# Optimization experiments

Hardware: AMD Instinct MI355X
Metric: run time of the kernel (lower is better)

The kernel has to match this reference:

```python
import jax, jax.numpy as jnp
import numpy as np

B, DAYS, N, E = 2, 8, 10000, 80000
C_IN, C_OUT, H = 32, 32, 4
NEG_SLOPE = 0.2


def setup_inputs() -> dict:
    key = jax.random.key(0)
    ks = jax.random.split(key, 7)
    x = jax.random.randint(ks[0], (B, DAYS, N), 0, N)
    adjacency = jax.random.randint(ks[1], (2, E), 0, N)
    embedding = jax.random.normal(ks[2], (N, C_IN), dtype=jnp.float32)
    # GATConv linear: in_channels -> heads*out_channels
    W = jax.random.normal(ks[3], (C_IN, H * C_OUT), dtype=jnp.float32) / np.sqrt(C_IN)
    att_src = jax.random.normal(ks[4], (H, C_OUT), dtype=jnp.float32) / np.sqrt(C_OUT)
    att_dst = jax.random.normal(ks[5], (H, C_OUT), dtype=jnp.float32) / np.sqrt(C_OUT)
    bias = jnp.zeros((H * C_OUT,), dtype=jnp.float32)
    return {"x": x, "adjacency": adjacency, "embedding": embedding,
            "W": W, "att_src": att_src, "att_dst": att_dst, "bias": bias}


def _gat_forward(feat, src, dst, W, att_src, att_dst, bias):
    # feat: [G, N, C_IN]; same edge list shared across the G graphs
    G = feat.shape[0]
    xh = (feat @ W).reshape(G, N, H, C_OUT)              # [G,N,H,C]
    a_src = jnp.einsum('gnhc,hc->gnh', xh, att_src)       # [G,N,H]
    a_dst = jnp.einsum('gnhc,hc->gnh', xh, att_dst)
    alpha = a_src[:, src] + a_dst[:, dst]                 # [G,Et,H]
    alpha = jnp.where(alpha >= 0, alpha, NEG_SLOPE * alpha)

    def per_graph(al, msgs):
        # segment softmax over incoming edges of each dst node
        m = jax.ops.segment_max(al, dst, num_segments=N)  # [N,H]
        e = jnp.exp(al - m[dst])                          # [Et,H]
        s = jax.ops.segment_sum(e, dst, num_segments=N)
        w = e / (s[dst] + 1e-16)
        out = jax.ops.segment_sum(w[..., None] * msgs, dst, num_segments=N)
        return out                                        # [N,H,C]

    out = jax.vmap(per_graph)(alpha, xh[:, src])          # [G,N,H,C]
    return out.reshape(G, N, H * C_OUT) + bias


def reference(x, adjacency, embedding, W, att_src, att_dst, bias):
    Bd, Dd = x.shape[0], x.shape[1]
    feat = embedding[x].reshape(-1, N, C_IN)              # [G,N,C_IN]
    # GATConv default add_self_loops=True
    loops = jnp.arange(N, dtype=adjacency.dtype)
    src = jnp.concatenate([adjacency[0], loops])
    dst = jnp.concatenate([adjacency[1], loops])
    out = _gat_forward(feat, src, dst, W, att_src, att_dst, bias)
    return out.reshape(Bd, Dd, -1)
```

## Files before the change

kernel.cpp:

```cpp
#include <hip/hip_runtime.h>
#include <hip/hip_bf16.h>
#include <math.h>

#define C_IN 32
#define H 4
#define C_OUT 32
#define HC (H * C_OUT)
#define NEG_SLOPE 0.2f
#define CSR_STRIDE 64

typedef float v2f __attribute__((ext_vector_type(2)));

#define RPB 16
__global__ __launch_bounds__(256) void build_kernel(
        const int* __restrict__ adj, int E, int N,
        int* __restrict__ deg, int* __restrict__ csr,
        const float* __restrict__ emb, const float* __restrict__ W,
        const float* __restrict__ att_src, const float* __restrict__ att_dst,
        __hip_bfloat16* __restrict__ T, float* __restrict__ ta_src,
        float* __restrict__ ta_dst, int tblocks) {
    if ((int)blockIdx.x >= tblocks) {
        int e = (blockIdx.x - tblocks) * 256 + threadIdx.x;
        int Et = E + N;
        if (e < Et) {
            int s = (e < E) ? adj[e] : (e - E);
            int d = (e < E) ? adj[E + e] : (e - E);
            int pos = atomicAdd(&deg[d], 1);
            if (pos < CSR_STRIDE) csr[(d << 6) + pos] = s;
        }
        return;
    }
    int t = threadIdx.x;
    int sub = t >> 7;
    int tc = t & 127;
    int h = tc >> 5, c = tc & 31;
    int base = blockIdx.x * RPB;
    int nmax = (N - base < RPB) ? (N - base) : RPB;

    float wcol[C_IN];
#pragma unroll
    for (int k = 0; k < C_IN; k++) wcol[k] = W[k * HC + tc];
    float as = att_src[h * C_OUT + c];
    float adw = att_dst[h * C_OUT + c];

    for (int it = sub; it < nmax; it += 2) {
        int r = __builtin_amdgcn_readfirstlane(base + it);
        const float* ep = emb + (size_t)r * C_IN;
        float acc = 0.f;
#pragma unroll
        for (int k = 0; k < C_IN; k++) acc += ep[k] * wcol[k];
        T[(size_t)r * HC + tc] = __float2bfloat16(acc);
        float ps = acc * as, pd = acc * adw;
#pragma unroll
        for (int o = 16; o; o >>= 1) {
            ps += __shfl_xor(ps, o, 32);
            pd += __shfl_xor(pd, o, 32);
        }
        if (c == 0) {
            ta_src[r * H + h] = ps;
            ta_dst[r * H + h] = pd;
        }
    }
}

__global__ __launch_bounds__(256) void agg_kernel(
        const int* __restrict__ deg, const int* __restrict__ csr,
        const int* __restrict__ x, const unsigned int* __restrict__ Tu,
        const float* __restrict__ ta_src, const float* __restrict__ ta_dst,
        const float* __restrict__ bias, float* __restrict__ out, int N, int G) {
    __shared__ int xs8_lds[16][69];

    int t = threadIdx.x;
    int n = blockIdx.x;
    int dg = deg[n];
    if (dg > CSR_STRIDE) dg = CSR_STRIDE;
    int dgp4 = (dg + 3) & ~3;
    const int* cb = csr + (n << 6);

    {
        int gA = t >> 4;
        int e0 = t & 15;
        const int* xg = x + (size_t)gA * N;
        for (int c0 = 0; c0 < dg; c0 += 16) {
            int slot = c0 + e0;
            int sv = cb[slot];
            int s = (slot < dg) ? sv : 0;
            xs8_lds[gA][slot] = xg[s] << 8;
        }
    }
    __syncthreads();

    int wid = t >> 6;
    int lane = t & 63;
    int lg = lane >> 4;
    int li = lane & 15;
    int gj = wid * 4 + lg;
    int hh = li >> 2;
    unsigned int li16 = (unsigned int)(li << 4);

    int xgn = x[(size_t)gj * N + n];
    float ad = ta_dst[xgn * H + hh];

    v2f a0 = {0.f, 0.f}, a1 = {0.f, 0.f}, a2 = {0.f, 0.f}, a3 = {0.f, 0.f};
    float dsum = 0.f;

#pragma unroll 4
    for (int e = 0; e < dgp4; e++) {
        int xs8 = xs8_lds[gj][e];
        int xs = xs8 >> 8;
        float a = ta_src[xs * H + hh] + ad;
        a = fmaxf(a, NEG_SLOPE * a);
        float w = (e < dg) ? __expf(a) : 0.f;
        uint4 u = *(const uint4*)((const char*)Tu + (unsigned int)xs8 + li16);
        v2f w2 = {w, w};
        v2f t0 = {__uint_as_float(u.x << 16), __uint_as_float(u.x & 0xffff0000u)};
        v2f t1 = {__uint_as_float(u.y << 16), __uint_as_float(u.y & 0xffff0000u)};
        v2f t2 = {__uint_as_float(u.z << 16), __uint_as_float(u.z & 0xffff0000u)};
        v2f t3 = {__uint_as_float(u.w << 16), __uint_as_float(u.w & 0xffff0000u)};
        a0 += w2 * t0;
        a1 += w2 * t1;
        a2 += w2 * t2;
        a3 += w2 * t3;
        dsum += w;
    }

    float inv = __builtin_amdgcn_rcpf(dsum + 1e-16f);
    const float4* bp = (const float4*)(bias + li * 8);
    float4 b0 = bp[0], b1 = bp[1];
    float4 o0 = {a0.x * inv + b0.x, a0.y * inv + b0.y,
                 a1.x * inv + b0.z, a1.y * inv + b0.w};
    float4 o1 = {a2.x * inv + b1.x, a2.y * inv + b1.y,
                 a3.x * inv + b1.z, a3.y * inv + b1.w};
    float* op = out + (size_t)gj * N * HC + (size_t)n * HC + li * 8;
    *(float4*)op = o0;
    *(float4*)(op + 4) = o1;
}

extern "C" void kernel_launch(void* const* d_in, const int* in_sizes, int n_in,
                              void* d_out, int out_size, void* d_ws, size_t ws_size,
                              hipStream_t stream) {
    const int*   x       = (const int*)d_in[0];
    const int*   adj     = (const int*)d_in[1];
    const float* emb     = (const float*)d_in[2];
    const float* W       = (const float*)d_in[3];
    const float* att_src = (const float*)d_in[4];
    const float* att_dst = (const float*)d_in[5];
    const float* bias    = (const float*)d_in[6];
    float* out = (float*)d_out;

    const int N  = in_sizes[2] / C_IN;
    const int GN = in_sizes[0];
    const int G  = GN / N;
    const int E  = in_sizes[1] / 2;
    const int Et = E + N;

    char* ws = (char*)d_ws;
    size_t o = 0;
    auto carve = [&](size_t bytes) -> void* {
        void* p = ws + o;
        o = (o + bytes + 255) & ~(size_t)255;
        return p;
    };
    __hip_bfloat16* T = (__hip_bfloat16*)carve((size_t)N * HC * sizeof(__hip_bfloat16));
    float* ta_src  = (float*)carve((size_t)N * H * sizeof(float));
    float* ta_dst  = (float*)carve((size_t)N * H * sizeof(float));
    int*   deg     = (int*)carve((size_t)N * sizeof(int));
    int*   csr     = (int*)carve((size_t)N * CSR_STRIDE * sizeof(int));

    hipMemsetAsync(deg, 0, (size_t)N * sizeof(int), stream);

    int tblocks = (N + RPB - 1) / RPB;
    int fblocks = (Et + 255) / 256;
    build_kernel<<<tblocks + fblocks, 256, 0, stream>>>(
        adj, E, N, deg, csr, emb, W, att_src, att_dst, T, ta_src, ta_dst, tblocks);

    agg_kernel<<<N, 256, 0, stream>>>(deg, csr, x,
                                      (const unsigned int*)T, ta_src, ta_dst,
                                      bias, out, N, G);
}
```

Baseline: 147.6 us.

## Precompute per-graph source attention table and hoist edge weights into LDS

Adds a prep kernel that packs each node's shifted embedding index and its four source attention logits (as fp16) into one int4 entry per graph node. In the aggregation kernel, the staging phase now computes all four heads' leaky-relu and exp weights per edge once and stores them in LDS. This replaces the per-lane dependent gathers of ta_src and the repeated exp in the inner loop, which were duplicated across the four lanes that share a head. The cost is an extra kernel launch, an extra 16-byte-per-node table in global memory, more LDS use, and fp16 rounding of the source logits.

```diff
diff --git a/kernel.cpp b/kernel.cpp
--- a/kernel.cpp
+++ b/kernel.cpp
@@ -1,5 +1,6 @@
 #include <hip/hip_runtime.h>
 #include <hip/hip_bf16.h>
+#include <hip/hip_fp16.h>
 #include <math.h>
 
 #define C_IN 32
@@ -63,12 +64,29 @@
     }
 }
 
+__global__ __launch_bounds__(256) void prep_kernel(
+        const int* __restrict__ x, const float* __restrict__ ta_src,
+        int4* __restrict__ as_tab, int GN) {
+    int idx = blockIdx.x * 256 + threadIdx.x;
+    if (idx >= GN) return;
+    int xs = x[idx];
+    float4 tv = *(const float4*)(ta_src + xs * H);
+    __half2 p01 = __floats2half2_rn(tv.x, tv.y);
+    __half2 p23 = __floats2half2_rn(tv.z, tv.w);
+    union { __half2 h; int i; } u01, u23;
+    u01.h = p01; u23.h = p23;
+    int4 ent = { xs << 8, u01.i, u23.i, 0 };
+    as_tab[idx] = ent;
+}
+
 __global__ __launch_bounds__(256) void agg_kernel(
         const int* __restrict__ deg, const int* __restrict__ csr,
-        const int* __restrict__ x, const unsigned int* __restrict__ Tu,
-        const float* __restrict__ ta_src, const float* __restrict__ ta_dst,
+        const int* __restrict__ x, const int4* __restrict__ as_tab,
+        const unsigned int* __restrict__ Tu,
+        const float* __restrict__ ta_dst,
         const float* __restrict__ bias, float* __restrict__ out, int N, int G) {
-    __shared__ int xs8_lds[16][69];
+    __shared__ float4 w4_lds[16][65];
+    __shared__ int    xs8_lds[16][65];
 
     int t = threadIdx.x;
     int n = blockIdx.x;
@@ -78,14 +96,34 @@
     const int* cb = csr + (n << 6);
 
     {
-        int gA = t >> 4;
+        int g = t >> 4;
         int e0 = t & 15;
-        const int* xg = x + (size_t)gA * N;
+        int xgn = x[(size_t)g * N + n];
+        float4 adv = *(const float4*)(ta_dst + xgn * H);
+        const int4* ag = as_tab + (size_t)g * N;
         for (int c0 = 0; c0 < dg; c0 += 16) {
             int slot = c0 + e0;
             int sv = cb[slot];
             int s = (slot < dg) ? sv : 0;
-            xs8_lds[gA][slot] = xg[s] << 8;
+            int4 ent = ag[s];
+            union { int i; __half2 h; } q01, q23;
+            q01.i = ent.y; q23.i = ent.z;
+            float2 t01 = __half22float2(q01.h);
+            float2 t23 = __half22float2(q23.h);
+            float a0 = t01.x + adv.x, a1 = t01.y + adv.y;
+            float a2 = t23.x + adv.z, a3 = t23.y + adv.w;
+            a0 = fmaxf(a0, NEG_SLOPE * a0);
+            a1 = fmaxf(a1, NEG_SLOPE * a1);
+            a2 = fmaxf(a2, NEG_SLOPE * a2);
+            a3 = fmaxf(a3, NEG_SLOPE * a3);
+            float4 w4;
+            if (slot < dg) {
+                w4 = (float4){__expf(a0), __expf(a1), __expf(a2), __expf(a3)};
+            } else {
+                w4 = (float4){0.f, 0.f, 0.f, 0.f};
+            }
+            w4_lds[g][slot] = w4;
+            xs8_lds[g][slot] = ent.x;
         }
     }
     __syncthreads();
@@ -98,19 +136,13 @@
     int hh = li >> 2;
     unsigned int li16 = (unsigned int)(li << 4);
 
-    int xgn = x[(size_t)gj * N + n];
-    float ad = ta_dst[xgn * H + hh];
-
     v2f a0 = {0.f, 0.f}, a1 = {0.f, 0.f}, a2 = {0.f, 0.f}, a3 = {0.f, 0.f};
     float dsum = 0.f;
 
 #pragma unroll 4
     for (int e = 0; e < dgp4; e++) {
         int xs8 = xs8_lds[gj][e];
-        int xs = xs8 >> 8;
-        float a = ta_src[xs * H + hh] + ad;
-        a = fmaxf(a, NEG_SLOPE * a);
-        float w = (e < dg) ? __expf(a) : 0.f;
+        float w = ((const float*)&w4_lds[gj][e])[hh];
         uint4 u = *(const uint4*)((const char*)Tu + (unsigned int)xs8 + li16);
         v2f w2 = {w, w};
         v2f t0 = {__uint_as_float(u.x << 16), __uint_as_float(u.x & 0xffff0000u)};
@@ -166,6 +198,7 @@
     float* ta_dst  = (float*)carve((size_t)N * H * sizeof(float));
     int*   deg     = (int*)carve((size_t)N * sizeof(int));
     int*   csr     = (int*)carve((size_t)N * CSR_STRIDE * sizeof(int));
+    int4*  as_tab  = (int4*)carve((size_t)GN * sizeof(int4));
 
     hipMemsetAsync(deg, 0, (size_t)N * sizeof(int), stream);
 
@@ -174,7 +207,9 @@
     build_kernel<<<tblocks + fblocks, 256, 0, stream>>>(
         adj, E, N, deg, csr, emb, W, att_src, att_dst, T, ta_src, ta_dst, tblocks);
 
-    agg_kernel<<<N, 256, 0, stream>>>(deg, csr, x,
-                                      (const unsigned int*)T, ta_src, ta_dst,
+    prep_kernel<<<(GN + 255) / 256, 256, 0, stream>>>(x, ta_src, as_tab, GN);
+
+    agg_kernel<<<N, 256, 0, stream>>>(deg, csr, x, as_tab,
+                                      (const unsigned int*)T, ta_dst,
                                       bias, out, N, G);
 }
```

After: 156.5 us. 1.06x slower.
